# Performance work log

Hardware: AMD Instinct MI355X
Metric: run time of the kernel (lower is better)

The kernel has to match this reference:

```python
import jax, jax.numpy as jnp
import numpy as np

B, C_IN, H, W = 32, 3, 48, 48
CONV_DIM = 64
HID = 128
N_CLASSES = 10
SP_PER_IMG = 144            # superpixels per image (48*48 / 16 pixels each)
N1 = B * H * W              # pixel-graph nodes = 73728
E1 = 8 * N1                 # pixel-graph edges
G = B * SP_PER_IMG          # superpixel-graph nodes = 4608
E2 = 16 * G                 # superpixel-graph edges
EPS = 1e-5


def setup_inputs() -> dict:
    key = jax.random.key(0)
    ks = jax.random.split(key, 16)
    images = jax.random.normal(ks[0], (B, C_IN, H, W), jnp.float32)

    # (img_idx, h, w) for every pixel node
    idx = np.arange(N1)
    pdw = np.stack([idx // (H * W), (idx // W) % H, idx % W], axis=1).astype(np.int64)
    pixel_data_where = jnp.asarray(pdw)

    # pixel-graph edges, intra-image
    rs = np.random.RandomState(1)
    src_l = rs.randint(0, H * W, E1)
    dst_l = rs.randint(0, H * W, E1)
    img_e = np.arange(E1) % B
    pixel_edge_index = jnp.asarray(
        np.stack([img_e * (H * W) + src_l, img_e * (H * W) + dst_l]).astype(np.int64))

    # pixel node -> superpixel id (16 pixels per superpixel)
    pixel_batch = jnp.asarray(((idx // (H * W)) * SP_PER_IMG + (idx % (H * W)) // 16).astype(np.int64))

    # superpixel-graph edges, intra-image
    gsrc_l = rs.randint(0, SP_PER_IMG, E2)
    gdst_l = rs.randint(0, SP_PER_IMG, E2)
    gimg = np.arange(E2) % B
    graph_edge_index = jnp.asarray(
        np.stack([gimg * SP_PER_IMG + gsrc_l, gimg * SP_PER_IMG + gdst_l]).astype(np.int64))

    # superpixel -> image id
    graph_batch = jnp.asarray((np.arange(G) // SP_PER_IMG).astype(np.int64))

    def rn(k, shape, fan_in):
        return jax.random.normal(k, shape, jnp.float32) / np.sqrt(fan_in)

    params = dict(
        conv_w=rn(ks[1], (CONV_DIM, C_IN), C_IN),
        conv_b=jnp.zeros((CONV_DIM,), jnp.float32),
        emb1_W=rn(ks[2], (CONV_DIM, HID), CONV_DIM),
        emb1_b=jnp.zeros((HID,), jnp.float32),
        gcn1_W=rn(ks[3], (2, HID, HID), HID),
        gcn1_b=jnp.zeros((2, HID), jnp.float32),
        bn1_g=jnp.ones((2, HID), jnp.float32),
        bn1_b=jnp.zeros((2, HID), jnp.float32),
        emb2_W=rn(ks[4], (HID, HID), HID),
        emb2_b=jnp.zeros((HID,), jnp.float32),
        gcn2_W=rn(ks[5], (2, HID, HID), HID),
        gcn2_b=jnp.zeros((2, HID), jnp.float32),
        bn2_g=jnp.ones((2, HID), jnp.float32),
        bn2_b=jnp.zeros((2, HID), jnp.float32),
        readout_W=rn(ks[6], (HID, N_CLASSES), HID),
    )
    return dict(images=images, pixel_data_where=pixel_data_where,
                pixel_edge_index=pixel_edge_index, pixel_batch=pixel_batch,
                graph_edge_index=graph_edge_index, graph_batch=graph_batch, **params)


def _gcn_conv(x, Wt, b, src, dst, n):
    # PyG GCNConv, normalize=True: x@W, add self-loops, sym deg-norm, scatter-add, +bias
    x = x @ Wt
    loops = jnp.arange(n)
    s = jnp.concatenate([src, loops])
    d = jnp.concatenate([dst, loops])
    deg = jax.ops.segment_sum(jnp.ones(s.shape[0], x.dtype), d, num_segments=n)
    dinv = jnp.where(deg > 0, jax.lax.rsqrt(jnp.maximum(deg, 1e-12)), 0.0)
    norm = dinv[s] * dinv[d]
    out = jax.ops.segment_sum(x[s] * norm[:, None], d, num_segments=n)
    return out + b


def _bn(x, g, b):
    m = x.mean(0)
    v = x.var(0)
    return (x - m) * jax.lax.rsqrt(v + EPS) * g + b


def _mean_pool(x, seg, n):
    s = jax.ops.segment_sum(x, seg, num_segments=n)
    c = jax.ops.segment_sum(jnp.ones(x.shape[0], x.dtype), seg, num_segments=n)
    return s / jnp.maximum(c, 1.0)[:, None]


def reference(images, pixel_data_where, pixel_edge_index, pixel_batch,
              graph_edge_index, graph_batch,
              conv_w, conv_b, emb1_W, emb1_b, gcn1_W, gcn1_b, bn1_g, bn1_b,
              emb2_W, emb2_b, gcn2_W, gcn2_b, bn2_g, bn2_b, readout_W):
    # CONVNet: 1x1 conv + ReLU
    feat = jnp.einsum('bchw,oc->bohw', images, conv_w) + conv_b[None, :, None, None]
    feat = jax.nn.relu(feat)
    # gather per-pixel node features: [N1, CONV_DIM]
    px = feat[pixel_data_where[:, 0], :, pixel_data_where[:, 1], pixel_data_where[:, 2]]

    # GCNNet1 on pixel graph
    h = px @ emb1_W + emb1_b
    for i in range(2):
        h_in = h
        h = _gcn_conv(h_in, gcn1_W[i], gcn1_b[i],
                      pixel_edge_index[0], pixel_edge_index[1], N1)
        h = jax.nn.relu(_bn(h, bn1_g[i], bn1_b[i]))
        h = h_in + h  # residual (dims match)
    hg = _mean_pool(h, pixel_batch, G)  # [G, HID]

    # GCNNet2 on superpixel graph
    h2 = hg @ emb2_W + emb2_b
    for i in range(2):
        h_in = h2
        h2 = _gcn_conv(h_in, gcn2_W[i], gcn2_b[i],
                       graph_edge_index[0], graph_edge_index[1], G)
        h2 = jax.nn.relu(_bn(h2, bn2_g[i], bn2_b[i]))
        h2 = h_in + h2
    hg2 = _mean_pool(h2, graph_batch, B)  # [B, HID]
    logits = hg2 @ readout_W              # [B, N_CLASSES], readout has no bias
    return logits
```

## Files before the change

kernel.cpp:

```cpp
#include <hip/hip_runtime.h>

typedef unsigned short u16;
typedef unsigned int u32;
typedef __attribute__((ext_vector_type(8))) short short8;
typedef __attribute__((ext_vector_type(4))) float f32x4;

constexpr int kB   = 32;
constexpr int kN1 = 73728;
constexpr int kE1 = 589824;
constexpr int kG  = 4608;
constexpr int kE2 = 73728;
constexpr float kEPS = 1e-5f;

__device__ inline u16 f2bf(float f) {
  unsigned u = __float_as_uint(f);
  return (u16)((u + 0x7fffu + ((u >> 16) & 1u)) >> 16);
}
__device__ inline float bflo(u32 v) { return __uint_as_float(v << 16); }
__device__ inline float bfhi(u32 v) { return __uint_as_float(v & 0xffff0000u); }
__device__ inline u32 pack2(float a, float b) {
  return (u32)f2bf(a) | ((u32)f2bf(b) << 16);
}

__global__ void prep_kernel(const float* __restrict__ e1w, const float* __restrict__ g1w,
                            const float* __restrict__ e2w, const float* __restrict__ g2w,
                            u16* __restrict__ Wt,
                            const int* __restrict__ s1, const int* __restrict__ d1,
                            const int* __restrict__ s2, const int* __restrict__ d2,
                            u32* __restrict__ ep1, u32* __restrict__ ep2,
                            float* __restrict__ sums) {
  int i = blockIdx.x * 256 + threadIdx.x;
  if (i < 90112) {
    if (i < 8192) {
      int k = i >> 7, n = i & 127;
      Wt[n * 64 + k] = f2bf(e1w[i]);
    } else if (i < 40960) {
      int j = i - 8192;
      int mat = j >> 14, jj = j & 16383;
      int k = jj >> 7, n = jj & 127;
      Wt[8192 + mat * 16384 + n * 128 + k] = f2bf(g1w[j]);
    } else if (i < 57344) {
      int j = i - 40960;
      int k = j >> 7, n = j & 127;
      Wt[40960 + n * 128 + k] = f2bf(e2w[j]);
    } else {
      int j = i - 57344;
      int mat = j >> 14, jj = j & 16383;
      int k = jj >> 7, n = jj & 127;
      Wt[57344 + mat * 16384 + n * 128 + k] = f2bf(g2w[j]);
    }
    return;
  }
  int e = i - 90112;
  if (e < kE1) {
    int b = e & 31;
    u32 sl = (u32)(s1[e] - b * 2304);
    u32 dl = (u32)(d1[e] - b * 2304);
    ep1[b * 18432 + (e >> 5)] = (sl << 12) | dl;
    return;
  }
  e -= kE1;
  if (e < kE2) {
    int b = e & 31;
    u32 sl = (u32)(s2[e] - b * 144);
    u32 dl = (u32)(d2[e] - b * 144);
    ep2[b * 2304 + (e >> 5)] = (sl << 8) | dl;
    return;
  }
  e -= kE2;
  if (e < 1024) sums[e] = 0.f;
}

__global__ __launch_bounds__(1024) void csr_build_kernel(
    const u32* __restrict__ ep1, int* __restrict__ rp1, int* __restrict__ col1,
    float* __restrict__ dinv1,
    const u32* __restrict__ ep2, int* __restrict__ rp2, int* __restrict__ col2,
    float* __restrict__ dinv2) {
  __shared__ int cnt[2304];
  __shared__ int pref[2304];
  __shared__ int wsum[16];
  __shared__ int carry;
  int tid = threadIdx.x;
  int lane = tid & 63, w = tid >> 6;
  int b = blockIdx.x & 31;
  bool g1 = blockIdx.x < 32;
  const u32* ep = g1 ? ep1 + b * 18432 : ep2 + b * 2304;
  int ne    = g1 ? 18432 : 2304;
  int nv    = g1 ? 2304 : 144;
  int ebase = g1 ? b * 18432 : b * 2304;
  int vbase = g1 ? b * 2304 : b * 144;
  int* rp    = g1 ? rp1 : rp2;
  int* col   = g1 ? col1 : col2;
  float* dnv = g1 ? dinv1 : dinv2;
  int shift = g1 ? 12 : 8;
  int mask = (1 << shift) - 1;

  for (int v = tid; v < nv; v += 1024) cnt[v] = 0;
  if (tid == 0) carry = 0;
  __syncthreads();
  for (int e = tid; e < ne; e += 1024) atomicAdd(&cnt[ep[e] & mask], 1);
  __syncthreads();

  for (int base = 0; base < nv; base += 1024) {
    int idx = base + tid;
    int v = (idx < nv) ? cnt[idx] : 0;
    int inc = v;
#pragma unroll
    for (int off = 1; off < 64; off <<= 1) {
      int t = __shfl_up(inc, off, 64);
      if (lane >= off) inc += t;
    }
    if (lane == 63) wsum[w] = inc;
    __syncthreads();
    if (w == 0) {
      int t = (lane < 16) ? wsum[lane] : 0;
#pragma unroll
      for (int off = 1; off < 16; off <<= 1) {
        int u2 = __shfl_up(t, off, 64);
        if (lane >= off) t += u2;
      }
      if (lane < 16) wsum[lane] = t;
    }
    __syncthreads();
    int woff = (w > 0) ? wsum[w - 1] : 0;
    if (idx < nv) pref[idx] = carry + woff + inc - v;
    __syncthreads();
    if (tid == 0) carry += wsum[15];
    __syncthreads();
  }

  for (int v = tid; v < nv; v += 1024) {
    rp[vbase + v] = ebase + pref[v];
    dnv[vbase + v] = rsqrtf((float)(cnt[v] + 1));
  }
  if (blockIdx.x == 31 && tid == 0) rp1[kN1] = kE1;
  if (blockIdx.x == 63 && tid == 0) rp2[kG] = kE2;

  for (int v = tid; v < nv; v += 1024) cnt[v] = pref[v];
  __syncthreads();
  for (int e = tid; e < ne; e += 1024) {
    u32 pk = ep[e];
    int dl = pk & mask, sl = (int)(pk >> shift);
    int p = atomicAdd(&cnt[dl], 1);
    col[ebase + p] = vbase + sl;
  }
}

__device__ __forceinline__ void mfma_body128(const u16* As, const u16* Bs,
                                             const float* __restrict__ bias,
                                             u16* __restrict__ Cb, int row0) {
  int tid = threadIdx.x;
  int wid = tid >> 6, lane = tid & 63;
  int lr = lane & 15, lg = lane >> 4;
  f32x4 acc[2][8];
#pragma unroll
  for (int m = 0; m < 2; m++)
#pragma unroll
    for (int n = 0; n < 8; n++) acc[m][n] = (f32x4){0.f, 0.f, 0.f, 0.f};
#pragma unroll
  for (int kk = 0; kk < 4; ++kk) {
    short8 a[2];
#pragma unroll
    for (int m = 0; m < 2; ++m) {
      int r = wid * 32 + m * 16 + lr;
      int c = (kk * 4 + lg) ^ (r & 7);
      a[m] = *reinterpret_cast<const short8*>(&As[r * 128 + c * 8]);
    }
#pragma unroll
    for (int n = 0; n < 8; ++n) {
      int rb = n * 16 + lr;
      int cb = (kk * 4 + lg) ^ (rb & 7);
      short8 b = *reinterpret_cast<const short8*>(&Bs[rb * 128 + cb * 8]);
      acc[0][n] = __builtin_amdgcn_mfma_f32_16x16x32_bf16(a[0], b, acc[0][n], 0, 0, 0);
      acc[1][n] = __builtin_amdgcn_mfma_f32_16x16x32_bf16(a[1], b, acc[1][n], 0, 0, 0);
    }
  }
#pragma unroll
  for (int m = 0; m < 2; ++m)
#pragma unroll
    for (int n = 0; n < 8; ++n) {
      int col = n * 16 + lr;
      float bv = bias ? bias[col] : 0.f;
#pragma unroll
      for (int j = 0; j < 4; ++j) {
        int row = row0 + wid * 32 + m * 16 + lg * 4 + j;
        Cb[(size_t)row * 128 + col] = f2bf(acc[m][n][j] + bv);
      }
    }
}

__global__ __launch_bounds__(256) void gemm_conv2(
    const float* __restrict__ img, const float* __restrict__ cw,
    const float* __restrict__ cb, const u16* __restrict__ WtE1,
    const float* __restrict__ emb1b, const u16* __restrict__ WtG10,
    u16* __restrict__ h_out, u16* __restrict__ x_out) {
  __shared__ __align__(16) char smem[65536];
  u16* As1 = (u16*)smem;
  u16* Bs1 = (u16*)(smem + 16384);
  float* wls = (float*)(smem + 32768);
  u16* As2 = (u16*)smem;
  u16* Bs2 = (u16*)(smem + 32768);
  int tid = threadIdx.x;
  int row0 = blockIdx.x * 128;
  int b = row0 / 2304;

  if (tid < 192) wls[tid] = cw[tid];
  else if (tid < 256) wls[tid] = cb[tid - 192];
  for (int i = tid; i < 128 * 8; i += 256) {
    int r = i >> 3, c = i & 7;
    int cs = c ^ (r & 7);
    *reinterpret_cast<float4*>(&Bs1[r * 64 + cs * 8]) =
        *reinterpret_cast<const float4*>(&WtE1[r * 64 + c * 8]);
  }
  __syncthreads();

  {
    int r = tid >> 1, hf = tid & 1;
    int rem = row0 + r - b * 2304;
    int hh = rem / 48, ww = rem - hh * 48;
    const float* ib = img + ((size_t)(b * 3) * 48 + hh) * 48 + ww;
    float i0 = ib[0], i1 = ib[2304], i2 = ib[4608];
#pragma unroll
    for (int cc = 0; cc < 4; ++cc) {
      int c = hf * 4 + cc;
      u32 packed[4];
#pragma unroll
      for (int u = 0; u < 4; ++u) {
        int c0 = c * 8 + u * 2;
        float a0 = wls[192 + c0];
        a0 = fmaf(i0, wls[c0 * 3 + 0], a0);
        a0 = fmaf(i1, wls[c0 * 3 + 1], a0);
        a0 = fmaf(i2, wls[c0 * 3 + 2], a0);
        float a1 = wls[192 + c0 + 1];
        a1 = fmaf(i0, wls[c0 * 3 + 3], a1);
        a1 = fmaf(i1, wls[c0 * 3 + 4], a1);
        a1 = fmaf(i2, wls[c0 * 3 + 5], a1);
        packed[u] = pack2(fmaxf(a0, 0.f), fmaxf(a1, 0.f));
      }
      int cs = c ^ (r & 7);
      *reinterpret_cast<float4*>(&As1[r * 64 + cs * 8]) =
          *reinterpret_cast<const float4*>(packed);
    }
  }
  __syncthreads();

  {
    int wid = tid >> 6, lane = tid & 63;
    int lr = lane & 15, lg = lane >> 4;
    f32x4 acc[2][8];
#pragma unroll
    for (int m = 0; m < 2; m++)
#pragma unroll
      for (int n = 0; n < 8; n++) acc[m][n] = (f32x4){0.f, 0.f, 0.f, 0.f};
#pragma unroll
    for (int kk = 0; kk < 2; ++kk) {
      short8 a[2];
#pragma unroll
      for (int m = 0; m < 2; ++m) {
        int r = wid * 32 + m * 16 + lr;
        int c = (kk * 4 + lg) ^ (r & 7);
        a[m] = *reinterpret_cast<const short8*>(&As1[r * 64 + c * 8]);
      }
#pragma unroll
      for (int n = 0; n < 8; ++n) {
        int rb = n * 16 + lr;
        int cbk = (kk * 4 + lg) ^ (rb & 7);
        short8 bb = *reinterpret_cast<const short8*>(&Bs1[rb * 64 + cbk * 8]);
        acc[0][n] = __builtin_amdgcn_mfma_f32_16x16x32_bf16(a[0], bb, acc[0][n], 0, 0, 0);
        acc[1][n] = __builtin_amdgcn_mfma_f32_16x16x32_bf16(a[1], bb, acc[1][n], 0, 0, 0);
      }
    }
#pragma unroll
    for (int m = 0; m < 2; ++m)
#pragma unroll
      for (int n = 0; n < 8; ++n) {
        int colx = n * 16 + lr;
        float bv = emb1b[colx];
#pragma unroll
        for (int j = 0; j < 4; ++j) {
          int row = row0 + wid * 32 + m * 16 + lg * 4 + j;
          h_out[(size_t)row * 128 + colx] = f2bf(acc[m][n][j] + bv);
        }
      }
  }
  __syncthreads();

  for (int i = tid; i < 128 * 16; i += 256) {
    int r = i >> 4, c = i & 15;
    int cs = c ^ (r & 7);
    *reinterpret_cast<float4*>(&As2[r * 128 + cs * 8]) =
        *reinterpret_cast<const float4*>(&h_out[(size_t)(row0 + r) * 128 + c * 8]);
    *reinterpret_cast<float4*>(&Bs2[r * 128 + cs * 8]) =
        *reinterpret_cast<const float4*>(&WtG10[(size_t)r * 128 + c * 8]);
  }
  __syncthreads();
  mfma_body128(As2, Bs2, nullptr, x_out, row0);
}

__global__ __launch_bounds__(256) void gemm_chain2(
    const u16* __restrict__ hg, const u16* __restrict__ WtE2,
    const float* __restrict__ emb2b, const u16* __restrict__ WtG20,
    u16* __restrict__ h2_out, u16* __restrict__ x2_out) {
  __shared__ __align__(16) char smem[65536];
  u16* As = (u16*)smem;
  u16* Bs = (u16*)(smem + 32768);
  int tid = threadIdx.x;
  int row0 = blockIdx.x * 128;

  for (int i = tid; i < 128 * 16; i += 256) {
    int r = i >> 4, c = i & 15;
    int cs = c ^ (r & 7);
    *reinterpret_cast<float4*>(&As[r * 128 + cs * 8]) =
        *reinterpret_cast<const float4*>(&hg[(size_t)(row0 + r) * 128 + c * 8]);
    *reinterpret_cast<float4*>(&Bs[r * 128 + cs * 8]) =
        *reinterpret_cast<const float4*>(&WtE2[(size_t)r * 128 + c * 8]);
  }
  __syncthreads();
  mfma_body128(As, Bs, emb2b, h2_out, row0);
  __syncthreads();

  for (int i = tid; i < 128 * 16; i += 256) {
    int r = i >> 4, c = i & 15;
    int cs = c ^ (r & 7);
    *reinterpret_cast<float4*>(&As[r * 128 + cs * 8]) =
        *reinterpret_cast<const float4*>(&h2_out[(size_t)(row0 + r) * 128 + c * 8]);
    *reinterpret_cast<float4*>(&Bs[r * 128 + cs * 8]) =
        *reinterpret_cast<const float4*>(&WtG20[(size_t)r * 128 + c * 8]);
  }
  __syncthreads();
  mfma_body128(As, Bs, nullptr, x2_out, row0);
}

__global__ __launch_bounds__(256) void gemm_apply(
    u32* __restrict__ h, const u32* __restrict__ agg, const float* __restrict__ sums,
    const float* __restrict__ g, const float* __restrict__ bb, float inv_n,
    const u16* __restrict__ Wt, u16* __restrict__ Cb) {
  __shared__ __align__(16) u16 As[128 * 128];
  __shared__ __align__(16) u16 Bs[128 * 128];
  __shared__ float scls[256];
  int tid = threadIdx.x;
  int row0 = blockIdx.x * 128;

  if (tid < 128) {
    float m = sums[tid] * inv_n;
    float var = sums[128 + tid] * inv_n - m * m;
    float sc = g[tid] * rsqrtf(var + kEPS);
    scls[tid] = sc;
    scls[128 + tid] = bb[tid] - m * sc;
  }
  __syncthreads();

  for (int i = tid; i < 128 * 16; i += 256) {
    int r = i >> 4, c = i & 15;
    int cs = c ^ (r & 7);
    *reinterpret_cast<float4*>(&Bs[r * 128 + cs * 8]) =
        *reinterpret_cast<const float4*>(&Wt[(size_t)r * 128 + c * 8]);
    size_t gidx = (size_t)(row0 + r) * 64 + c * 4;
    u32 hv4[4], av4[4], o[4];
    *reinterpret_cast<float4*>(hv4) = *reinterpret_cast<const float4*>(&h[gidx]);
    *reinterpret_cast<float4*>(av4) = *reinterpret_cast<const float4*>(&agg[gidx]);
#pragma unroll
    for (int u = 0; u < 4; ++u) {
      int f = c * 8 + u * 2;
      float x0 = fmaf(bflo(av4[u]), scls[f], scls[128 + f]);
      float x1 = fmaf(bfhi(av4[u]), scls[f + 1], scls[129 + f]);
      o[u] = pack2(bflo(hv4[u]) + fmaxf(x0, 0.f), bfhi(hv4[u]) + fmaxf(x1, 0.f));
    }
    *reinterpret_cast<float4*>(&As[r * 128 + cs * 8]) = *reinterpret_cast<const float4*>(o);
    *reinterpret_cast<float4*>(&h[gidx]) = *reinterpret_cast<const float4*>(o);
  }
  __syncthreads();
  mfma_body128(As, Bs, nullptr, Cb, row0);
}

__global__ __launch_bounds__(256) void agg_kernel(
    const u32* __restrict__ x, const int* __restrict__ rp,
    const int* __restrict__ col, const float* __restrict__ dinv,
    const float* __restrict__ bias, u32* __restrict__ out) {
  int nwg = gridDim.x;
  int chunk = nwg >> 3;
  int bid = blockIdx.x;
  int swz = (bid & 7) * chunk + (bid >> 3);
  int d = swz * 4 + (threadIdx.x >> 6);
  int f2 = threadIdx.x & 63;
  float dd = dinv[d];
  u32 v = x[(size_t)d * 64 + f2];
  float acc0 = bflo(v) * dd, acc1 = bfhi(v) * dd;
  int e = rp[d], end = rp[d + 1];
  for (; e + 3 < end; e += 4) {
    int s0 = col[e], s1 = col[e + 1], s2 = col[e + 2], s3 = col[e + 3];
    float d0 = dinv[s0], d1 = dinv[s1], d2 = dinv[s2], d3 = dinv[s3];
    u32 v0 = x[(size_t)s0 * 64 + f2];
    u32 v1 = x[(size_t)s1 * 64 + f2];
    u32 v2 = x[(size_t)s2 * 64 + f2];
    u32 v3 = x[(size_t)s3 * 64 + f2];
    acc0 = fmaf(bflo(v0), d0, acc0); acc1 = fmaf(bfhi(v0), d0, acc1);
    acc0 = fmaf(bflo(v1), d1, acc0); acc1 = fmaf(bfhi(v1), d1, acc1);
    acc0 = fmaf(bflo(v2), d2, acc0); acc1 = fmaf(bfhi(v2), d2, acc1);
    acc0 = fmaf(bflo(v3), d3, acc0); acc1 = fmaf(bfhi(v3), d3, acc1);
  }
  for (; e < end; ++e) {
    int s0 = col[e];
    float d0 = dinv[s0];
    u32 v0 = x[(size_t)s0 * 64 + f2];
    acc0 = fmaf(bflo(v0), d0, acc0); acc1 = fmaf(bfhi(v0), d0, acc1);
  }
  out[(size_t)d * 64 + f2] = pack2(acc0 * dd + bias[2 * f2], acc1 * dd + bias[2 * f2 + 1]);
}

__global__ __launch_bounds__(256) void bn_stats_kernel(const u32* __restrict__ x, int nrows,
                                                       float* __restrict__ sums) {
  __shared__ float red[1024];
  int tid = threadIdx.x;
  int f2 = tid & 63, half = tid >> 6;
  float s0 = 0.f, s1 = 0.f, q0 = 0.f, q1 = 0.f;
  for (int row = blockIdx.x * 4 + half; row < nrows; row += gridDim.x * 4) {
    u32 v = x[(size_t)row * 64 + f2];
    float a = bflo(v), b = bfhi(v);
    s0 += a; s1 += b;
    q0 = fmaf(a, a, q0); q1 = fmaf(b, b, q1);
  }
  red[tid] = s0; red[256 + tid] = s1; red[512 + tid] = q0; red[768 + tid] = q1;
  __syncthreads();
  if (half == 0) {
    float S0 = red[f2] + red[64 + f2] + red[128 + f2] + red[192 + f2];
    float S1 = red[256 + f2] + red[320 + f2] + red[384 + f2] + red[448 + f2];
    float Q0 = red[512 + f2] + red[576 + f2] + red[640 + f2] + red[704 + f2];
    float Q1 = red[768 + f2] + red[832 + f2] + red[896 + f2] + red[960 + f2];
    atomicAdd(&sums[2 * f2], S0);
    atomicAdd(&sums[2 * f2 + 1], S1);
    atomicAdd(&sums[128 + 2 * f2], Q0);
    atomicAdd(&sums[128 + 2 * f2 + 1], Q1);
  }
}

__global__ __launch_bounds__(256) void apply_pool1_kernel(
    const u32* __restrict__ h, const u32* __restrict__ agg,
    const float* __restrict__ sums, const float* __restrict__ g,
    const float* __restrict__ bb, float inv_n, u32* __restrict__ hg) {
  __shared__ float red[512];
  int gidx = blockIdx.x;
  int f2 = threadIdx.x & 63, half = threadIdx.x >> 6;
  int f = 2 * f2;
  float m0 = sums[f] * inv_n,     m1 = sums[f + 1] * inv_n;
  float v0 = sums[128 + f] * inv_n - m0 * m0;
  float v1 = sums[129 + f] * inv_n - m1 * m1;
  float sc0 = g[f] * rsqrtf(v0 + kEPS), sc1 = g[f + 1] * rsqrtf(v1 + kEPS);
  float sh0 = bb[f] - m0 * sc0, sh1 = bb[f + 1] - m1 * sc1;
  float s0 = 0.f, s1 = 0.f;
  int base = gidx * 16 + half * 4;
#pragma unroll
  for (int j = 0; j < 4; j++) {
    size_t idx = (size_t)(base + j) * 64 + f2;
    u32 av = agg[idx], hv = h[idx];
    float x0 = fmaf(bflo(av), sc0, sh0);
    float x1 = fmaf(bfhi(av), sc1, sh1);
    s0 += bflo(hv) + fmaxf(x0, 0.f);
    s1 += bfhi(hv) + fmaxf(x1, 0.f);
  }
  red[threadIdx.x] = s0; red[256 + threadIdx.x] = s1;
  __syncthreads();
  if (half == 0) {
    float S0 = red[f2] + red[64 + f2] + red[128 + f2] + red[192 + f2];
    float S1 = red[256 + f2] + red[320 + f2] + red[384 + f2] + red[448 + f2];
    hg[(size_t)gidx * 64 + f2] = pack2(S0 * (1.f / 16.f), S1 * (1.f / 16.f));
  }
}

__global__ __launch_bounds__(256) void graph_final(
    const u32* __restrict__ h2, const u32* __restrict__ agg2,
    const float* __restrict__ sums, const float* __restrict__ bn_g,
    const float* __restrict__ bn_b, float inv_n,
    const float* __restrict__ readW, float* __restrict__ out) {
  __shared__ float scls[256];
  __shared__ float red[512];
  __shared__ float hgrow[128];
  int tid = threadIdx.x, blk = blockIdx.x;
  if (tid < 128) {
    float m = sums[tid] * inv_n;
    float var = sums[128 + tid] * inv_n - m * m;
    float sc = bn_g[tid] * rsqrtf(var + kEPS);
    scls[tid] = sc;
    scls[128 + tid] = bn_b[tid] - m * sc;
  }
  __syncthreads();
  int f2 = tid & 63, w = tid >> 6;
  int f = 2 * f2;
  float sc0 = scls[f], sc1 = scls[f + 1];
  float sh0 = scls[128 + f], sh1 = scls[129 + f];
  float s0 = 0.f, s1 = 0.f;
  for (int it = 0; it < 36; ++it) {
    int row = blk * 144 + w * 36 + it;
    size_t idx = (size_t)row * 64 + f2;
    u32 av = agg2[idx], hv = h2[idx];
    float x0 = fmaf(bflo(av), sc0, sh0);
    float x1 = fmaf(bfhi(av), sc1, sh1);
    s0 += bflo(hv) + fmaxf(x0, 0.f);
    s1 += bfhi(hv) + fmaxf(x1, 0.f);
  }
  red[tid] = s0; red[256 + tid] = s1;
  __syncthreads();
  if (w == 0) {
    float S0 = red[f2] + red[64 + f2] + red[128 + f2] + red[192 + f2];
    float S1 = red[256 + f2] + red[320 + f2] + red[384 + f2] + red[448 + f2];
    hgrow[f]     = S0 * (1.f / 144.f);
    hgrow[f + 1] = S1 * (1.f / 144.f);
  }
  __syncthreads();
  if (tid < 10) {
    float acc = 0.f;
#pragma unroll 4
    for (int k = 0; k < 128; ++k) acc = fmaf(hgrow[k], readW[k * 10 + tid], acc);
    out[blk * 10 + tid] = acc;
  }
}

extern "C" void kernel_launch(void* const* d_in, const int* in_sizes, int n_in,
                              void* d_out, int out_size, void* d_ws, size_t ws_size,
                              hipStream_t stream) {
  const float* images  = (const float*)d_in[0];
  const int*   pei     = (const int*)d_in[2];
  const int*   gei     = (const int*)d_in[4];
  const float* conv_w  = (const float*)d_in[6];
  const float* conv_b  = (const float*)d_in[7];
  const float* emb1_W  = (const float*)d_in[8];
  const float* emb1_b  = (const float*)d_in[9];
  const float* gcn1_W  = (const float*)d_in[10];
  const float* gcn1_b  = (const float*)d_in[11];
  const float* bn1_g   = (const float*)d_in[12];
  const float* bn1_b   = (const float*)d_in[13];
  const float* emb2_W  = (const float*)d_in[14];
  const float* emb2_b  = (const float*)d_in[15];
  const float* gcn2_W  = (const float*)d_in[16];
  const float* gcn2_b  = (const float*)d_in[17];
  const float* bn2_g   = (const float*)d_in[18];
  const float* bn2_b   = (const float*)d_in[19];
  const float* readW   = (const float*)d_in[20];
  float* out = (float*)d_out;

  const int* src1 = pei;
  const int* dst1 = pei + kE1;
  const int* src2 = gei;
  const int* dst2 = gei + kE2;

  size_t off = 0;
  auto alloc = [&](size_t bytes) -> void* {
    void* p = (char*)d_ws + off;
    off += (bytes + 255) & ~(size_t)255;
    return p;
  };
  u32* hbf  = (u32*)alloc((size_t)kN1 * 64 * 4);
  u32* xbf  = (u32*)alloc((size_t)kN1 * 64 * 4);
  u32* aggb = (u32*)alloc((size_t)kN1 * 64 * 4);
  u32* ep1  = (u32*)alloc((size_t)kE1 * 4);
  u32* ep2  = (u32*)alloc((size_t)kE2 * 4);
  int*   rp1  = (int*)alloc((size_t)(kN1 + 1) * 4);
  float* dinv1 = (float*)alloc((size_t)kN1 * 4);
  int*   col1 = (int*)alloc((size_t)kE1 * 4);
  int*   rp2  = (int*)alloc((size_t)(kG + 1) * 4);
  float* dinv2 = (float*)alloc((size_t)kG * 4);
  int*   col2 = (int*)alloc((size_t)kE2 * 4);
  float* sums  = (float*)alloc(1024 * 4);
  u16*   Wt    = (u16*)alloc(90112 * 2);
  u32*   hgbf  = (u32*)alloc((size_t)kG * 64 * 4);
  u32*   h2bf  = (u32*)alloc((size_t)kG * 64 * 4);
  u32*   x2bf  = (u32*)alloc((size_t)kG * 64 * 4);
  u32*   agg2b = (u32*)alloc((size_t)kG * 64 * 4);

  float* ss0 = sums, *ss1 = sums + 256, *ss2 = sums + 512, *ss3 = sums + 768;

  const u16* WT_E1  = Wt + 0;
  const u16* WT_G10 = Wt + 8192;
  const u16* WT_G11 = Wt + 24576;
  const u16* WT_E2  = Wt + 40960;
  const u16* WT_G20 = Wt + 57344;
  const u16* WT_G21 = Wt + 73728;

  const float invN1 = 1.f / (float)kN1, invG = 1.f / (float)kG;

  prep_kernel<<<2948, 256, 0, stream>>>(emb1_W, gcn1_W, emb2_W, gcn2_W, Wt,
                                        src1, dst1, src2, dst2, ep1, ep2, sums);
  csr_build_kernel<<<64, 1024, 0, stream>>>(ep1, rp1, col1, dinv1, ep2, rp2, col2, dinv2);

  gemm_conv2<<<kN1 / 128, 256, 0, stream>>>(images, conv_w, conv_b, WT_E1, emb1_b,
                                            WT_G10, (u16*)hbf, (u16*)xbf);

  agg_kernel<<<kN1 / 4, 256, 0, stream>>>(xbf, rp1, col1, dinv1, gcn1_b, aggb);
  bn_stats_kernel<<<576, 256, 0, stream>>>(aggb, kN1, ss0);

  gemm_apply<<<kN1 / 128, 256, 0, stream>>>(hbf, aggb, ss0, bn1_g, bn1_b, invN1,
                                            WT_G11, (u16*)xbf);
  agg_kernel<<<kN1 / 4, 256, 0, stream>>>(xbf, rp1, col1, dinv1, gcn1_b + 128, aggb);
  bn_stats_kernel<<<576, 256, 0, stream>>>(aggb, kN1, ss1);
  apply_pool1_kernel<<<kG, 256, 0, stream>>>(hbf, aggb, ss1, bn1_g + 128, bn1_b + 128,
                                             invN1, hgbf);

  gemm_chain2<<<kG / 128, 256, 0, stream>>>((const u16*)hgbf, WT_E2, emb2_b, WT_G20,
                                            (u16*)h2bf, (u16*)x2bf);
  agg_kernel<<<kG / 4, 256, 0, stream>>>(x2bf, rp2, col2, dinv2, gcn2_b, agg2b);
  bn_stats_kernel<<<72, 256, 0, stream>>>(agg2b, kG, ss2);
  gemm_apply<<<kG / 128, 256, 0, stream>>>(h2bf, agg2b, ss2, bn2_g, bn2_b, invG,
                                           WT_G21, (u16*)x2bf);
  agg_kernel<<<kG / 4, 256, 0, stream>>>(x2bf, rp2, col2, dinv2, gcn2_b + 128, agg2b);
  bn_stats_kernel<<<72, 256, 0, stream>>>(agg2b, kG, ss3);
  graph_final<<<kB, 256, 0, stream>>>(h2bf, agg2b, ss3, bn2_g + 128, bn2_b + 128,
                                      invG, readW, out);
}
```

Baseline: 272.5 us.

## Merge prep and CSR build; fuse graph-2 aggregation with BN statistics

Removes the intermediate packed edge arrays by building the CSR directly from the strided source/destination index arrays inside a merged prep kernel. CSR blocks now use 256 threads instead of 1024, and the weight conversion runs in extra blocks of the same launch. For the superpixel graph, aggregation and batch-norm statistics are fused into one 1024-thread kernel, so two kernel launches and a re-read of the aggregate are dropped. The trade-off is fewer threads per CSR block and strided, uncoalesced index reads, which may lengthen the CSR phase.

```diff
diff --git a/kernel.cpp b/kernel.cpp
--- a/kernel.cpp
+++ b/kernel.cpp
@@ -22,15 +22,18 @@
   return (u32)f2bf(a) | ((u32)f2bf(b) << 16);
 }
 
-__global__ void prep_kernel(const float* __restrict__ e1w, const float* __restrict__ g1w,
-                            const float* __restrict__ e2w, const float* __restrict__ g2w,
-                            u16* __restrict__ Wt,
-                            const int* __restrict__ s1, const int* __restrict__ d1,
-                            const int* __restrict__ s2, const int* __restrict__ d2,
-                            u32* __restrict__ ep1, u32* __restrict__ ep2,
-                            float* __restrict__ sums) {
-  int i = blockIdx.x * 256 + threadIdx.x;
-  if (i < 90112) {
+__global__ __launch_bounds__(256) void prep_csr_kernel(
+    const float* __restrict__ e1w, const float* __restrict__ g1w,
+    const float* __restrict__ e2w, const float* __restrict__ g2w,
+    u16* __restrict__ Wt,
+    const int* __restrict__ s1, const int* __restrict__ d1,
+    const int* __restrict__ s2, const int* __restrict__ d2,
+    int* __restrict__ rp1, int* __restrict__ col1, float* __restrict__ dinv1,
+    int* __restrict__ rp2, int* __restrict__ col2, float* __restrict__ dinv2,
+    float* __restrict__ sums) {
+  int tid = threadIdx.x;
+  if (blockIdx.x >= 64) {
+    int i = (blockIdx.x - 64) * 256 + tid;
     if (i < 8192) {
       int k = i >> 7, n = i & 127;
       Wt[n * 64 + k] = f2bf(e1w[i]);
@@ -43,65 +46,43 @@
       int j = i - 40960;
       int k = j >> 7, n = j & 127;
       Wt[40960 + n * 128 + k] = f2bf(e2w[j]);
-    } else {
+    } else if (i < 90112) {
       int j = i - 57344;
       int mat = j >> 14, jj = j & 16383;
       int k = jj >> 7, n = jj & 127;
       Wt[57344 + mat * 16384 + n * 128 + k] = f2bf(g2w[j]);
+    } else {
+      sums[i - 90112] = 0.f;
     }
     return;
   }
-  int e = i - 90112;
-  if (e < kE1) {
-    int b = e & 31;
-    u32 sl = (u32)(s1[e] - b * 2304);
-    u32 dl = (u32)(d1[e] - b * 2304);
-    ep1[b * 18432 + (e >> 5)] = (sl << 12) | dl;
-    return;
-  }
-  e -= kE1;
-  if (e < kE2) {
-    int b = e & 31;
-    u32 sl = (u32)(s2[e] - b * 144);
-    u32 dl = (u32)(d2[e] - b * 144);
-    ep2[b * 2304 + (e >> 5)] = (sl << 8) | dl;
-    return;
-  }
-  e -= kE2;
-  if (e < 1024) sums[e] = 0.f;
-}
-
-__global__ __launch_bounds__(1024) void csr_build_kernel(
-    const u32* __restrict__ ep1, int* __restrict__ rp1, int* __restrict__ col1,
-    float* __restrict__ dinv1,
-    const u32* __restrict__ ep2, int* __restrict__ rp2, int* __restrict__ col2,
-    float* __restrict__ dinv2) {
+
   __shared__ int cnt[2304];
   __shared__ int pref[2304];
-  __shared__ int wsum[16];
+  __shared__ int wsum[4];
+  __shared__ int wpre[4];
   __shared__ int carry;
-  int tid = threadIdx.x;
   int lane = tid & 63, w = tid >> 6;
-  int b = blockIdx.x & 31;
-  bool g1 = blockIdx.x < 32;
-  const u32* ep = g1 ? ep1 + b * 18432 : ep2 + b * 2304;
-  int ne    = g1 ? 18432 : 2304;
-  int nv    = g1 ? 2304 : 144;
-  int ebase = g1 ? b * 18432 : b * 2304;
-  int vbase = g1 ? b * 2304 : b * 144;
+  int blk = blockIdx.x;
+  int b = blk & 31;
+  bool g1 = blk < 32;
+  const int* src = g1 ? s1 : s2;
+  const int* dst = g1 ? d1 : d2;
+  int ne = g1 ? 18432 : 2304;
+  int nv = g1 ? 2304 : 144;
+  int eb = g1 ? b * 18432 : b * 2304;
+  int vb = g1 ? b * 2304 : b * 144;
   int* rp    = g1 ? rp1 : rp2;
   int* col   = g1 ? col1 : col2;
   float* dnv = g1 ? dinv1 : dinv2;
-  int shift = g1 ? 12 : 8;
-  int mask = (1 << shift) - 1;
-
-  for (int v = tid; v < nv; v += 1024) cnt[v] = 0;
+
+  for (int v = tid; v < nv; v += 256) cnt[v] = 0;
   if (tid == 0) carry = 0;
   __syncthreads();
-  for (int e = tid; e < ne; e += 1024) atomicAdd(&cnt[ep[e] & mask], 1);
-  __syncthreads();
-
-  for (int base = 0; base < nv; base += 1024) {
+  for (int j = tid; j < ne; j += 256) atomicAdd(&cnt[dst[b + 32 * j] - vb], 1);
+  __syncthreads();
+
+  for (int base = 0; base < nv; base += 256) {
     int idx = base + tid;
     int v = (idx < nv) ? cnt[idx] : 0;
     int inc = v;
@@ -112,37 +93,31 @@
     }
     if (lane == 63) wsum[w] = inc;
     __syncthreads();
-    if (w == 0) {
-      int t = (lane < 16) ? wsum[lane] : 0;
-#pragma unroll
-      for (int off = 1; off < 16; off <<= 1) {
-        int u2 = __shfl_up(t, off, 64);
-        if (lane >= off) t += u2;
-      }
-      if (lane < 16) wsum[lane] = t;
+    if (tid == 0) {
+      int acc = carry;
+      for (int j = 0; j < 4; ++j) { wpre[j] = acc; acc += wsum[j]; }
+      carry = acc;
     }
     __syncthreads();
-    int woff = (w > 0) ? wsum[w - 1] : 0;
-    if (idx < nv) pref[idx] = carry + woff + inc - v;
+    if (idx < nv) pref[idx] = wpre[w] + inc - v;
     __syncthreads();
-    if (tid == 0) carry += wsum[15];
-    __syncthreads();
-  }
-
-  for (int v = tid; v < nv; v += 1024) {
-    rp[vbase + v] = ebase + pref[v];
-    dnv[vbase + v] = rsqrtf((float)(cnt[v] + 1));
-  }
-  if (blockIdx.x == 31 && tid == 0) rp1[kN1] = kE1;
-  if (blockIdx.x == 63 && tid == 0) rp2[kG] = kE2;
-
-  for (int v = tid; v < nv; v += 1024) cnt[v] = pref[v];
-  __syncthreads();
-  for (int e = tid; e < ne; e += 1024) {
-    u32 pk = ep[e];
-    int dl = pk & mask, sl = (int)(pk >> shift);
+  }
+
+  for (int v = tid; v < nv; v += 256) {
+    rp[vb + v] = eb + pref[v];
+    dnv[vb + v] = rsqrtf((float)(cnt[v] + 1));
+  }
+  if (blk == 31 && tid == 0) rp1[kN1] = kE1;
+  if (blk == 63 && tid == 0) rp2[kG] = kE2;
+
+  for (int v = tid; v < nv; v += 256) cnt[v] = pref[v];
+  __syncthreads();
+  for (int j = tid; j < ne; j += 256) {
+    int e = b + 32 * j;
+    int dl = dst[e] - vb;
+    int sl = src[e] - vb;
     int p = atomicAdd(&cnt[dl], 1);
-    col[ebase + p] = vbase + sl;
+    col[eb + p] = vb + sl;
   }
 }
 
@@ -434,6 +409,63 @@
   }
 }
 
+__global__ __launch_bounds__(1024) void agg_bn2_kernel(
+    const u32* __restrict__ x, const int* __restrict__ rp,
+    const int* __restrict__ col, const float* __restrict__ dinv,
+    const float* __restrict__ bias, u32* __restrict__ out,
+    float* __restrict__ sums) {
+  __shared__ float red[4096];
+  int nwg = gridDim.x;
+  int chunk = nwg >> 3;
+  int bid = blockIdx.x;
+  int swz = (bid & 7) * chunk + (bid >> 3);
+  int tid = threadIdx.x;
+  int w = tid >> 6, f2 = tid & 63;
+  int d = swz * 16 + w;
+  float dd = dinv[d];
+  u32 v = x[(size_t)d * 64 + f2];
+  float acc0 = bflo(v) * dd, acc1 = bfhi(v) * dd;
+  int e = rp[d], end = rp[d + 1];
+  for (; e + 3 < end; e += 4) {
+    int s0 = col[e], s1 = col[e + 1], s2 = col[e + 2], s3 = col[e + 3];
+    float d0 = dinv[s0], d1 = dinv[s1], d2 = dinv[s2], d3 = dinv[s3];
+    u32 v0 = x[(size_t)s0 * 64 + f2];
+    u32 v1 = x[(size_t)s1 * 64 + f2];
+    u32 v2 = x[(size_t)s2 * 64 + f2];
+    u32 v3 = x[(size_t)s3 * 64 + f2];
+    acc0 = fmaf(bflo(v0), d0, acc0); acc1 = fmaf(bfhi(v0), d0, acc1);
+    acc0 = fmaf(bflo(v1), d1, acc0); acc1 = fmaf(bfhi(v1), d1, acc1);
+    acc0 = fmaf(bflo(v2), d2, acc0); acc1 = fmaf(bfhi(v2), d2, acc1);
+    acc0 = fmaf(bflo(v3), d3, acc0); acc1 = fmaf(bfhi(v3), d3, acc1);
+  }
+  for (; e < end; ++e) {
+    int s0 = col[e];
+    float d0 = dinv[s0];
+    u32 v0 = x[(size_t)s0 * 64 + f2];
+    acc0 = fmaf(bflo(v0), d0, acc0); acc1 = fmaf(bfhi(v0), d0, acc1);
+  }
+  u32 pk = pack2(acc0 * dd + bias[2 * f2], acc1 * dd + bias[2 * f2 + 1]);
+  out[(size_t)d * 64 + f2] = pk;
+  float r0 = bflo(pk), r1 = bfhi(pk);
+  red[tid] = r0; red[1024 + tid] = r1;
+  red[2048 + tid] = r0 * r0; red[3072 + tid] = r1 * r1;
+  __syncthreads();
+  if (tid < 64) {
+    float S0 = 0.f, S1 = 0.f, Q0 = 0.f, Q1 = 0.f;
+#pragma unroll
+    for (int j = 0; j < 16; ++j) {
+      S0 += red[j * 64 + f2];
+      S1 += red[1024 + j * 64 + f2];
+      Q0 += red[2048 + j * 64 + f2];
+      Q1 += red[3072 + j * 64 + f2];
+    }
+    atomicAdd(&sums[2 * f2], S0);
+    atomicAdd(&sums[2 * f2 + 1], S1);
+    atomicAdd(&sums[128 + 2 * f2], Q0);
+    atomicAdd(&sums[128 + 2 * f2 + 1], Q1);
+  }
+}
+
 __global__ __launch_bounds__(256) void apply_pool1_kernel(
     const u32* __restrict__ h, const u32* __restrict__ agg,
     const float* __restrict__ sums, const float* __restrict__ g,
@@ -552,8 +584,6 @@
   u32* hbf  = (u32*)alloc((size_t)kN1 * 64 * 4);
   u32* xbf  = (u32*)alloc((size_t)kN1 * 64 * 4);
   u32* aggb = (u32*)alloc((size_t)kN1 * 64 * 4);
-  u32* ep1  = (u32*)alloc((size_t)kE1 * 4);
-  u32* ep2  = (u32*)alloc((size_t)kE2 * 4);
   int*   rp1  = (int*)alloc((size_t)(kN1 + 1) * 4);
   float* dinv1 = (float*)alloc((size_t)kN1 * 4);
   int*   col1 = (int*)alloc((size_t)kE1 * 4);
@@ -578,9 +608,9 @@
 
   const float invN1 = 1.f / (float)kN1, invG = 1.f / (float)kG;
 
-  prep_kernel<<<2948, 256, 0, stream>>>(emb1_W, gcn1_W, emb2_W, gcn2_W, Wt,
-                                        src1, dst1, src2, dst2, ep1, ep2, sums);
-  csr_build_kernel<<<64, 1024, 0, stream>>>(ep1, rp1, col1, dinv1, ep2, rp2, col2, dinv2);
+  prep_csr_kernel<<<420, 256, 0, stream>>>(emb1_W, gcn1_W, emb2_W, gcn2_W, Wt,
+                                           src1, dst1, src2, dst2,
+                                           rp1, col1, dinv1, rp2, col2, dinv2, sums);
 
   gemm_conv2<<<kN1 / 128, 256, 0, stream>>>(images, conv_w, conv_b, WT_E1, emb1_b,
                                             WT_G10, (u16*)hbf, (u16*)xbf);
@@ -597,12 +627,11 @@
 
   gemm_chain2<<<kG / 128, 256, 0, stream>>>((const u16*)hgbf, WT_E2, emb2_b, WT_G20,
                                             (u16*)h2bf, (u16*)x2bf);
-  agg_kernel<<<kG / 4, 256, 0, stream>>>(x2bf, rp2, col2, dinv2, gcn2_b, agg2b);
-  bn_stats_kernel<<<72, 256, 0, stream>>>(agg2b, kG, ss2);
+  agg_bn2_kernel<<<kG / 16, 1024, 0, stream>>>(x2bf, rp2, col2, dinv2, gcn2_b, agg2b, ss2);
   gemm_apply<<<kG / 128, 256, 0, stream>>>(h2bf, agg2b, ss2, bn2_g, bn2_b, invG,
                                            WT_G21, (u16*)x2bf);
-  agg_kernel<<<kG / 4, 256, 0, stream>>>(x2bf, rp2, col2, dinv2, gcn2_b + 128, agg2b);
-  bn_stats_kernel<<<72, 256, 0, stream>>>(agg2b, kG, ss3);
+  agg_bn2_kernel<<<kG / 16, 1024, 0, stream>>>(x2bf, rp2, col2, dinv2, gcn2_b + 128,
+                                               agg2b, ss3);
   graph_final<<<kB, 256, 0, stream>>>(h2bf, agg2b, ss3, bn2_g + 128, bn2_b + 128,
                                       invG, readW, out);
 }
```

Result: slower. 338.1 us (+24.1%).
